# Kernel optimization log

Hardware: AMD Instinct MI355X
Metric: run time of the kernel (lower is better)

## Reference

```python
import jax, jax.numpy as jnp
import numpy as np

N_SPECIES = 2
N_RBF = 16
HIDDEN = 64
CUTOFF = 2.5


def setup_inputs() -> dict:
    key = jax.random.key(0)
    ks = jax.random.split(key, 10)
    B, N = 8, 1024
    positions = jax.random.uniform(ks[0], (B, N, 3), dtype=jnp.float32) * 10.0
    types = jax.random.randint(ks[1], (B, N), 0, N_SPECIES)
    in_dim = N_SPECIES + N_SPECIES * N_RBF  # 34
    def lin(k, fan_in, fan_out):
        bound = 1.0 / np.sqrt(fan_in)
        kw, kb = jax.random.split(k)
        W = jax.random.uniform(kw, (fan_in, fan_out), minval=-bound, maxval=bound, dtype=jnp.float32)
        b = jax.random.uniform(kb, (fan_out,), minval=-bound, maxval=bound, dtype=jnp.float32)
        return W, b
    W1, b1 = lin(ks[2], in_dim, 64)
    W2, b2 = lin(ks[3], 64, 64)
    W3, b3 = lin(ks[4], 64, HIDDEN)
    return {"positions": positions, "types": types,
            "W1": W1, "b1": b1, "W2": W2, "b2": b2, "W3": W3, "b3": b3}


def _forward(positions, types, W1, b1, W2, b2, W3, b3):
    B, N, _ = positions.shape
    # pairwise distances with safe sqrt (zero grad on diagonal, matching torch norm subgradient)
    disp = positions[:, :, None, :] - positions[:, None, :, :]          # [B,N,N,3]
    sq = jnp.sum(disp * disp, axis=-1)                                   # [B,N,N]
    nz = sq > 0.0
    d = jnp.sqrt(jnp.where(nz, sq, 1.0)) * nz
    # RBF expansion
    centers = jnp.linspace(0.0, CUTOFF, N_RBF)
    widths = jnp.full((N_RBF,), CUTOFF / max(N_RBF - 1, 1))
    diff = d[..., None] - centers                                        # [B,N,N,R]
    rbf = jnp.exp(-(diff ** 2) / (widths ** 2 + 1e-12))
    # smooth polynomial cutoff
    x = d / CUTOFF
    cut = jnp.where(d < CUTOFF, 1.0 - 6.0 * x ** 5 + 15.0 * x ** 4 - 10.0 * x ** 3, 0.0)
    rbf = rbf * cut[..., None]
    eye = jnp.eye(N, dtype=bool)[None, :, :, None]
    rbf = jnp.where(eye, 0.0, rbf)
    # species-weighted neighbor aggregation
    onehot = jax.nn.one_hot(types, N_SPECIES, dtype=positions.dtype)      # [B,N,S]
    env = jnp.einsum('bijr,bjs->birs', rbf, onehot).reshape(B, N, -1)     # [B,N,R*S]
    feats = jnp.concatenate([onehot, env], axis=-1)                       # [B,N,S+S*R]
    h = jax.nn.silu(feats @ W1 + b1)
    h = jax.nn.silu(h @ W2 + b2)
    return h @ W3 + b3                                                    # [B,N,HIDDEN]


def reference(positions, types, W1, b1, W2, b2, W3, b3):
    return _forward(positions, types, W1, b1, W2, b2, W3, b3)
```

## Files before the change

kernel.cpp:

```cpp
#include <hip/hip_runtime.h>
#include <hip/hip_bf16.h>

#define NTHREADS 256
#define N_ATOMS 1024
#define HIDDEN 64

__global__ __launch_bounds__(NTHREADS) void LocalFeatureEncoder_40063454937486_kernel(
    const float* __restrict__ pos,
    const int*   __restrict__ types,
    const float* __restrict__ W1,
    const float* __restrict__ b1,
    const float* __restrict__ W2,
    const float* __restrict__ b2,
    const float* __restrict__ W3,
    const float* __restrict__ b3,
    float*       __restrict__ out)
{
    const int a    = blockIdx.x;
    const int bidx = a >> 10;
    const int i    = a & (N_ATOMS - 1);
    const int tid  = threadIdx.x;
    const int lane = tid & 63;
    const int wav  = tid >> 6;

    __shared__ float qd [N_ATOMS];
    __shared__ float qm0[N_ATOMS];
    __shared__ float qm1[N_ATOMS];
    __shared__ float partial[4 * 32];
    __shared__ float feats[64];
    __shared__ float h1s[64];
    __shared__ int   cnt;

    if (tid == 0) cnt = 0;

    const float* posb = pos + (size_t)bidx * N_ATOMS * 3;
    const int*   typb = types + (size_t)bidx * N_ATOMS;

    const float xi = posb[i * 3 + 0];
    const float yi = posb[i * 3 + 1];
    const float zi = posb[i * 3 + 2];

    __syncthreads();

#pragma unroll
    for (int it = 0; it < N_ATOMS / NTHREADS; ++it) {
        const int j = tid + it * NTHREADS;
        const float px = posb[j * 3 + 0];
        const float py = posb[j * 3 + 1];
        const float pz = posb[j * 3 + 2];
        const int   tj = typb[j];
        const float dx = xi - px, dy = yi - py, dz = zi - pz;
        const float sq = dx * dx + dy * dy + dz * dz;
        const bool pred = (j != i) && (sq < 6.25f);

        const unsigned long long mask = __ballot(pred);
        int base = 0;
        if (lane == 0 && mask) base = atomicAdd(&cnt, (int)__popcll(mask));
        base = __shfl(base, 0, 64);
        if (pred) {
            const float d  = sqrtf(sq);
            const float x  = d * 0.4f;
            const float x3 = x * x * x;
            const float cutv = 1.0f + x3 * (-10.0f + x * (15.0f - 6.0f * x));
            const int idx = base + (int)__popcll(mask & ((1ull << lane) - 1ull));
            qd [idx] = d;
            qm0[idx] = (tj == 0) ? cutv : 0.0f;
            qm1[idx] = (tj == 0) ? 0.0f : cutv;
        }
    }
    __syncthreads();
    const int n = cnt;

    const int p = tid >> 5;
    const int f = tid & 31;
    const int r = f >> 1;
    const int s = f & 1;
    const float c = (float)r * (2.5f / 15.0f);
    const float inv_w2 = 36.0f;
    const float* __restrict__ qm = (s == 0) ? qm0 : qm1;

    float acc = 0.0f;
    for (int e = p; e < n; e += 8) {
        const float d    = qd[e];
        const float m    = qm[e];
        const float diff = d - c;
        acc += m * __expf(-(diff * diff) * inv_w2);
    }
    acc += __shfl_xor(acc, 32, 64);
    if (lane < 32) partial[wav * 32 + f] = acc;
    if (tid == 0) {
        const int ti = typb[i];
        feats[0] = (ti == 0) ? 1.0f : 0.0f;
        feats[1] = (ti == 1) ? 1.0f : 0.0f;
    }
    __syncthreads();
    if (tid < 32)
        feats[2 + tid] = partial[tid] + partial[32 + tid] + partial[64 + tid] + partial[96 + tid];
    __syncthreads();

    if (tid < HIDDEN) {
        float h = b1[tid];
#pragma unroll
        for (int k = 0; k < 34; k++) h += feats[k] * W1[k * HIDDEN + tid];
        h = h / (1.0f + __expf(-h));
        h1s[tid] = h;
    }
    __syncthreads();
    if (tid < HIDDEN) {
        float h = b2[tid];
#pragma unroll
        for (int k = 0; k < HIDDEN; k++) h += h1s[k] * W2[k * HIDDEN + tid];
        h = h / (1.0f + __expf(-h));
        feats[tid] = h;
    }
    __syncthreads();
    if (tid < HIDDEN) {
        float o = b3[tid];
#pragma unroll
        for (int k = 0; k < HIDDEN; k++) o += feats[k] * W3[k * HIDDEN + tid];
        out[(size_t)a * HIDDEN + tid] = o;
    }
}

extern "C" void kernel_launch(void* const* d_in, const int* in_sizes, int n_in,
                              void* d_out, int out_size, void* d_ws, size_t ws_size,
                              hipStream_t stream) {
    const float* pos   = (const float*)d_in[0];
    const int*   types = (const int*)d_in[1];
    const float* W1    = (const float*)d_in[2];
    const float* b1    = (const float*)d_in[3];
    const float* W2    = (const float*)d_in[4];
    const float* b2    = (const float*)d_in[5];
    const float* W3    = (const float*)d_in[6];
    const float* b3    = (const float*)d_in[7];
    float*       out   = (float*)d_out;

    const int BN = in_sizes[1];

    LocalFeatureEncoder_40063454937486_kernel<<<BN, NTHREADS, 0, stream>>>(
        pos, types, W1, b1, W2, b2, W3, b3, out);
}
```

Before: 91.68 us.

## Map one atom per wavefront and keep neighbor data in registers

```diff
diff --git a/kernel.cpp b/kernel.cpp
--- a/kernel.cpp
+++ b/kernel.cpp
@@ -4,6 +4,10 @@
 #define NTHREADS 256
 #define N_ATOMS 1024
 #define HIDDEN 64
+
+__device__ __forceinline__ float rdlane(float v, int l) {
+    return __int_as_float(__builtin_amdgcn_readlane(__float_as_int(v), l));
+}
 
 __global__ __launch_bounds__(NTHREADS) void LocalFeatureEncoder_40063454937486_kernel(
     const float* __restrict__ pos,
@@ -16,22 +20,11 @@
     const float* __restrict__ b3,
     float*       __restrict__ out)
 {
-    const int a    = blockIdx.x;
+    const int tid  = threadIdx.x;
+    const int lane = tid & 63;
+    const int a    = blockIdx.x * 4 + (tid >> 6);
     const int bidx = a >> 10;
     const int i    = a & (N_ATOMS - 1);
-    const int tid  = threadIdx.x;
-    const int lane = tid & 63;
-    const int wav  = tid >> 6;
-
-    __shared__ float qd [N_ATOMS];
-    __shared__ float qm0[N_ATOMS];
-    __shared__ float qm1[N_ATOMS];
-    __shared__ float partial[4 * 32];
-    __shared__ float feats[64];
-    __shared__ float h1s[64];
-    __shared__ int   cnt;
-
-    if (tid == 0) cnt = 0;
 
     const float* posb = pos + (size_t)bidx * N_ATOMS * 3;
     const int*   typb = types + (size_t)bidx * N_ATOMS;
@@ -40,86 +33,92 @@
     const float yi = posb[i * 3 + 1];
     const float zi = posb[i * 3 + 2];
 
-    __syncthreads();
+    const int   r16 = lane & 15;
+    const int   slot = lane >> 4;
+    const float c    = (float)r16 * (2.5f / 15.0f);
+
+    float acc0 = 0.0f;
+    float acc1 = 0.0f;
 
 #pragma unroll
-    for (int it = 0; it < N_ATOMS / NTHREADS; ++it) {
-        const int j = tid + it * NTHREADS;
+    for (int sweep = 0; sweep < N_ATOMS / 64; ++sweep) {
+        const int j = lane + sweep * 64;
         const float px = posb[j * 3 + 0];
         const float py = posb[j * 3 + 1];
         const float pz = posb[j * 3 + 2];
         const int   tj = typb[j];
         const float dx = xi - px, dy = yi - py, dz = zi - pz;
         const float sq = dx * dx + dy * dy + dz * dz;
-        const bool pred = (j != i) && (sq < 6.25f);
+        const bool  pred = (j != i) && (sq < 6.25f);
 
-        const unsigned long long mask = __ballot(pred);
-        int base = 0;
-        if (lane == 0 && mask) base = atomicAdd(&cnt, (int)__popcll(mask));
-        base = __shfl(base, 0, 64);
+        float dv = 0.0f, mp = 0.0f;
         if (pred) {
             const float d  = sqrtf(sq);
             const float x  = d * 0.4f;
             const float x3 = x * x * x;
             const float cutv = 1.0f + x3 * (-10.0f + x * (15.0f - 6.0f * x));
-            const int idx = base + (int)__popcll(mask & ((1ull << lane) - 1ull));
-            qd [idx] = d;
-            qm0[idx] = (tj == 0) ? cutv : 0.0f;
-            qm1[idx] = (tj == 0) ? 0.0f : cutv;
+            dv = d;
+            mp = (tj == 0) ? cutv : -cutv;
+        }
+
+        unsigned long long mask = __ballot(pred);
+        while (mask) {
+            float dA = 0.0f, mA = 0.0f, dB = 0.0f, mB = 0.0f;
+            float dC = 0.0f, mC = 0.0f, dD = 0.0f, mD = 0.0f;
+            {
+                const int s = __builtin_ctzll(mask); mask &= mask - 1;
+                dA = rdlane(dv, s); mA = rdlane(mp, s);
+            }
+            if (mask) {
+                const int s = __builtin_ctzll(mask); mask &= mask - 1;
+                dB = rdlane(dv, s); mB = rdlane(mp, s);
+            }
+            if (mask) {
+                const int s = __builtin_ctzll(mask); mask &= mask - 1;
+                dC = rdlane(dv, s); mC = rdlane(mp, s);
+            }
+            if (mask) {
+                const int s = __builtin_ctzll(mask); mask &= mask - 1;
+                dD = rdlane(dv, s); mD = rdlane(mp, s);
+            }
+            const float d = (slot == 0) ? dA : (slot == 1) ? dB : (slot == 2) ? dC : dD;
+            const float m = (slot == 0) ? mA : (slot == 1) ? mB : (slot == 2) ? mC : dD == dD ? mD : mD;
+            const float diff = d - c;
+            const float e = __expf(diff * diff * -36.0f);
+            acc0 += e * fmaxf(m, 0.0f);
+            acc1 += e * fmaxf(-m, 0.0f);
         }
     }
-    __syncthreads();
-    const int n = cnt;
 
-    const int p = tid >> 5;
-    const int f = tid & 31;
-    const int r = f >> 1;
-    const int s = f & 1;
-    const float c = (float)r * (2.5f / 15.0f);
-    const float inv_w2 = 36.0f;
-    const float* __restrict__ qm = (s == 0) ? qm0 : qm1;
+    acc0 += __shfl_xor(acc0, 16, 64);
+    acc0 += __shfl_xor(acc0, 32, 64);
+    acc1 += __shfl_xor(acc1, 16, 64);
+    acc1 += __shfl_xor(acc1, 32, 64);
 
-    float acc = 0.0f;
-    for (int e = p; e < n; e += 8) {
-        const float d    = qd[e];
-        const float m    = qm[e];
-        const float diff = d - c;
-        acc += m * __expf(-(diff * diff) * inv_w2);
+    const int t  = lane;
+    const int ti = typb[i];
+
+    float h1 = b1[t] + W1[ti * HIDDEN + t];
+#pragma unroll
+    for (int r = 0; r < 16; ++r) {
+        h1 += rdlane(acc0, r) * W1[(2 + 2 * r + 0) * HIDDEN + t];
+        h1 += rdlane(acc1, r) * W1[(2 + 2 * r + 1) * HIDDEN + t];
     }
-    acc += __shfl_xor(acc, 32, 64);
-    if (lane < 32) partial[wav * 32 + f] = acc;
-    if (tid == 0) {
-        const int ti = typb[i];
-        feats[0] = (ti == 0) ? 1.0f : 0.0f;
-        feats[1] = (ti == 1) ? 1.0f : 0.0f;
+    h1 = h1 / (1.0f + __expf(-h1));
+
+    float h2 = b2[t];
+#pragma unroll
+    for (int k = 0; k < HIDDEN; ++k) {
+        h2 += rdlane(h1, k) * W2[k * HIDDEN + t];
     }
-    __syncthreads();
-    if (tid < 32)
-        feats[2 + tid] = partial[tid] + partial[32 + tid] + partial[64 + tid] + partial[96 + tid];
-    __syncthreads();
+    h2 = h2 / (1.0f + __expf(-h2));
 
-    if (tid < HIDDEN) {
-        float h = b1[tid];
+    float o = b3[t];
 #pragma unroll
-        for (int k = 0; k < 34; k++) h += feats[k] * W1[k * HIDDEN + tid];
-        h = h / (1.0f + __expf(-h));
-        h1s[tid] = h;
+    for (int k = 0; k < HIDDEN; ++k) {
+        o += rdlane(h2, k) * W3[k * HIDDEN + t];
     }
-    __syncthreads();
-    if (tid < HIDDEN) {
-        float h = b2[tid];
-#pragma unroll
-        for (int k = 0; k < HIDDEN; k++) h += h1s[k] * W2[k * HIDDEN + tid];
-        h = h / (1.0f + __expf(-h));
-        feats[tid] = h;
-    }
-    __syncthreads();
-    if (tid < HIDDEN) {
-        float o = b3[tid];
-#pragma unroll
-        for (int k = 0; k < HIDDEN; k++) o += feats[k] * W3[k * HIDDEN + tid];
-        out[(size_t)a * HIDDEN + tid] = o;
-    }
+    out[(size_t)a * HIDDEN + t] = o;
 }
 
 extern "C" void kernel_launch(void* const* d_in, const int* in_sizes, int n_in,
@@ -137,6 +136,6 @@
 
     const int BN = in_sizes[1];
 
-    LocalFeatureEncoder_40063454937486_kernel<<<BN, NTHREADS, 0, stream>>>(
+    LocalFeatureEncoder_40063454937486_kernel<<<BN / 4, NTHREADS, 0, stream>>>(
         pos, types, W1, b1, W2, b2, W3, b3, out);
 }
```

New measurement: 95.55 us. 4.2% more time.
